# Kernel tuning notes

Hardware: AMD Instinct MI355X
Metric: run time of the kernel (lower is better)

## Reference

```python
import jax, jax.numpy as jnp
import numpy as np

N, M, D = 8192, 8192, 64

def setup_inputs() -> dict:
    key = jax.random.key(0)
    kx, ky = jax.random.split(key)
    x = jax.random.normal(kx, (N, D), dtype=jnp.float32)
    y = jax.random.normal(ky, (M, D), dtype=jnp.float32)
    sigma = jnp.array(1.0, dtype=jnp.float32)
    return {"x": x, "y": y, "sigma": sigma}

def reference(x, y, sigma):
    # Flatten trailing dims (no-op here since inputs are already 2-D).
    x2 = x.reshape(x.shape[0], -1)
    y2 = y.reshape(y.shape[0], -1)
    # Pairwise squared distances via the GEMM trick:
    # |x_i - y_j|^2 = |x_i|^2 + |y_j|^2 - 2 x_i . y_j
    xn = jnp.sum(x2 * x2, axis=1)            # [N]
    yn = jnp.sum(y2 * y2, axis=1)            # [M]
    cross = x2 @ y2.T                         # [N, M]
    sqd = xn[:, None] + yn[None, :] - 2.0 * cross
    sqd = jnp.maximum(sqd, 0.0)               # clamp tiny negatives from fp error
    return jnp.exp(-0.5 * sqd / (sigma * sigma))  # [N, M]
```

## Files before the change

### kernel.cpp

```cpp
#include <hip/hip_runtime.h>
#include <hip/hip_bf16.h>

#define N 8192
#define M 8192
#define D 64

typedef __bf16 bf16x8 __attribute__((ext_vector_type(8)));
typedef float f32x4 __attribute__((ext_vector_type(4)));

__global__ __launch_bounds__(256) void prep_kernel(
    const float* __restrict__ x, const float* __restrict__ y,
    __bf16* __restrict__ xh, __bf16* __restrict__ xl, float* __restrict__ xn,
    __bf16* __restrict__ yh, __bf16* __restrict__ yl, float* __restrict__ yn)
{
    int row  = blockIdx.x * 4 + (threadIdx.x >> 6);
    int lane = threadIdx.x & 63;

    const float* src;
    __bf16 *h, *l;
    float* nrm;
    int r;
    if (row < N) { src = x; h = xh; l = xl; nrm = xn; r = row; }
    else         { src = y; h = yh; l = yl; nrm = yn; r = row - N; }

    float v = src[(size_t)r * D + lane];
    __bf16 hi = (__bf16)v;
    float  lof = v - (float)hi;
    __bf16 lo = (__bf16)lof;

    h[(size_t)r * D + lane] = hi;
    l[(size_t)r * D + lane] = lo;

    float s = v * v;
    #pragma unroll
    for (int off = 32; off; off >>= 1) s += __shfl_down(s, off, 64);
    if (lane == 0) nrm[r] = s;
}

__global__ __launch_bounds__(256) void rbf_kernel(
    const __bf16* __restrict__ xh, const __bf16* __restrict__ xl,
    const float* __restrict__ xn,
    const __bf16* __restrict__ yh, const __bf16* __restrict__ yl,
    const float* __restrict__ yn,
    const float* __restrict__ sig, float* __restrict__ out)
{
    int tid  = threadIdx.x;
    int wave = tid >> 6;
    int lane = tid & 63;
    int quad = lane >> 4;
    int l16  = lane & 15;

    int i_base = blockIdx.y * 128 + (wave >> 1) * 64;
    int j_base = blockIdx.x * 128 + (wave & 1) * 64;

    float s = sig[0];
    float scale = -0.5f / (s * s);

    bf16x8 Bh[4][2], Bl[4][2];
    float ynr[4];
    #pragma unroll
    for (int t = 0; t < 4; ++t) {
        int col = j_base + 4 * l16 + t;
        ynr[t] = yn[col];
        #pragma unroll
        for (int k = 0; k < 2; ++k) {
            int off = col * D + k * 32 + quad * 8;
            Bh[t][k] = *reinterpret_cast<const bf16x8*>(yh + off);
            Bl[t][k] = *reinterpret_cast<const bf16x8*>(yl + off);
        }
    }

    #pragma unroll
    for (int ti = 0; ti < 4; ++ti) {
        int arow = i_base + ti * 16 + l16;
        bf16x8 Ah[2], Al[2];
        #pragma unroll
        for (int k = 0; k < 2; ++k) {
            int off = arow * D + k * 32 + quad * 8;
            Ah[k] = *reinterpret_cast<const bf16x8*>(xh + off);
            Al[k] = *reinterpret_cast<const bf16x8*>(xl + off);
        }

        float xnr[4];
        #pragma unroll
        for (int r = 0; r < 4; ++r)
            xnr[r] = xn[i_base + ti * 16 + quad * 4 + r];

        f32x4 acc[4];
        #pragma unroll
        for (int t = 0; t < 4; ++t) acc[t] = (f32x4){0.f, 0.f, 0.f, 0.f};

        #pragma unroll
        for (int t = 0; t < 4; ++t) {
            #pragma unroll
            for (int k = 0; k < 2; ++k) {
                acc[t] = __builtin_amdgcn_mfma_f32_16x16x32_bf16(Ah[k], Bh[t][k], acc[t], 0, 0, 0);
                acc[t] = __builtin_amdgcn_mfma_f32_16x16x32_bf16(Ah[k], Bl[t][k], acc[t], 0, 0, 0);
                acc[t] = __builtin_amdgcn_mfma_f32_16x16x32_bf16(Al[k], Bh[t][k], acc[t], 0, 0, 0);
            }
        }

        #pragma unroll
        for (int r = 0; r < 4; ++r) {
            int row = i_base + ti * 16 + quad * 4 + r;
            f32x4 v;
            #pragma unroll
            for (int t = 0; t < 4; ++t) {
                float sqd = xnr[r] + ynr[t] - 2.0f * acc[t][r];
                sqd = fmaxf(sqd, 0.0f);
                v[t] = __expf(scale * sqd);
            }
            *reinterpret_cast<f32x4*>(out + (size_t)row * M + j_base + 4 * l16) = v;
        }
    }
}

extern "C" void kernel_launch(void* const* d_in, const int* in_sizes, int n_in,
                              void* d_out, int out_size, void* d_ws, size_t ws_size,
                              hipStream_t stream) {
    const float* x   = (const float*)d_in[0];
    const float* y   = (const float*)d_in[1];
    const float* sig = (const float*)d_in[2];
    float* out = (float*)d_out;

    char* ws = (char*)d_ws;
    __bf16* xh = (__bf16*)(ws);
    __bf16* xl = (__bf16*)(ws + (1u << 20));
    __bf16* yh = (__bf16*)(ws + (2u << 20));
    __bf16* yl = (__bf16*)(ws + (3u << 20));
    float*  xn = (float*) (ws + (4u << 20));
    float*  yn = (float*) (ws + (4u << 20) + (1u << 15));

    prep_kernel<<<(N + M) / 4, 256, 0, stream>>>(x, y, xh, xl, xn, yh, yl, yn);

    dim3 grid(M / 128, N / 128);
    rbf_kernel<<<grid, 256, 0, stream>>>(xh, xl, xn, yh, yl, yn, sig, out);
}
```

Baseline: 291.2 us.

## Pre-swizzle bf16 operands into MFMA fragment order and use nontemporal output stores

```diff
diff --git a/kernel.cpp b/kernel.cpp
--- a/kernel.cpp
+++ b/kernel.cpp
@@ -10,37 +10,56 @@
 
 __global__ __launch_bounds__(256) void prep_kernel(
     const float* __restrict__ x, const float* __restrict__ y,
-    __bf16* __restrict__ xh, __bf16* __restrict__ xl, float* __restrict__ xn,
-    __bf16* __restrict__ yh, __bf16* __restrict__ yl, float* __restrict__ yn)
+    __bf16* __restrict__ xsh, __bf16* __restrict__ xsl, float* __restrict__ xn,
+    __bf16* __restrict__ ysh, __bf16* __restrict__ ysl, float* __restrict__ yn)
 {
-    int row  = blockIdx.x * 4 + (threadIdx.x >> 6);
-    int lane = threadIdx.x & 63;
+    int t   = threadIdx.x;
+    int row = blockIdx.x * 32 + (t >> 3);
+    int c   = t & 7;
 
     const float* src;
-    __bf16 *h, *l;
+    __bf16 *ph, *pl;
     float* nrm;
     int r;
-    if (row < N) { src = x; h = xh; l = xl; nrm = xn; r = row; }
-    else         { src = y; h = yh; l = yl; nrm = yn; r = row - N; }
+    bool isx = row < N;
+    if (isx) { src = x; ph = xsh; pl = xsl; nrm = xn; r = row; }
+    else     { src = y; ph = ysh; pl = ysl; nrm = yn; r = row - N; }
 
-    float v = src[(size_t)r * D + lane];
-    __bf16 hi = (__bf16)v;
-    float  lof = v - (float)hi;
-    __bf16 lo = (__bf16)lof;
+    const float* p = src + (size_t)r * D + c * 8;
+    f32x4 a = *reinterpret_cast<const f32x4*>(p);
+    f32x4 b = *reinterpret_cast<const f32x4*>(p + 4);
+    float v[8] = {a[0], a[1], a[2], a[3], b[0], b[1], b[2], b[3]};
 
-    h[(size_t)r * D + lane] = hi;
-    l[(size_t)r * D + lane] = lo;
+    bf16x8 hv, lv;
+    float s = 0.0f;
+    #pragma unroll
+    for (int i = 0; i < 8; ++i) {
+        float vi = v[i];
+        __bf16 hi = (__bf16)vi;
+        float lof = vi - (float)hi;
+        hv[i] = hi;
+        lv[i] = (__bf16)lof;
+        s += vi * vi;
+    }
+    s += __shfl_down(s, 4);
+    s += __shfl_down(s, 2);
+    s += __shfl_down(s, 1);
 
-    float s = v * v;
-    #pragma unroll
-    for (int off = 32; off; off >>= 1) s += __shfl_down(s, off, 64);
-    if (lane == 0) nrm[r] = s;
+    int g = r >> 6, m = r & 63;
+    int slot;
+    if (isx) slot = ((m >> 4) * 2 + (c >> 2)) * 64 + (c & 3) * 16 + (m & 15);
+    else     slot = ((m & 3)  * 2 + (c >> 2)) * 64 + (c & 3) * 16 + (m >> 2);
+    size_t idx = (size_t)g * 4096 + (size_t)slot * 8;
+
+    *reinterpret_cast<bf16x8*>(ph + idx) = hv;
+    *reinterpret_cast<bf16x8*>(pl + idx) = lv;
+    if (c == 0) nrm[r] = s;
 }
 
 __global__ __launch_bounds__(256) void rbf_kernel(
-    const __bf16* __restrict__ xh, const __bf16* __restrict__ xl,
+    const __bf16* __restrict__ xsh, const __bf16* __restrict__ xsl,
     const float* __restrict__ xn,
-    const __bf16* __restrict__ yh, const __bf16* __restrict__ yl,
+    const __bf16* __restrict__ ysh, const __bf16* __restrict__ ysl,
     const float* __restrict__ yn,
     const float* __restrict__ sig, float* __restrict__ out)
 {
@@ -56,49 +75,43 @@
     float s = sig[0];
     float scale = -0.5f / (s * s);
 
+    const __bf16* pbh = ysh + (size_t)(j_base >> 6) * 4096 + lane * 8;
+    const __bf16* pbl = ysl + (size_t)(j_base >> 6) * 4096 + lane * 8;
     bf16x8 Bh[4][2], Bl[4][2];
-    float ynr[4];
     #pragma unroll
-    for (int t = 0; t < 4; ++t) {
-        int col = j_base + 4 * l16 + t;
-        ynr[t] = yn[col];
+    for (int t = 0; t < 4; ++t)
         #pragma unroll
         for (int k = 0; k < 2; ++k) {
-            int off = col * D + k * 32 + quad * 8;
-            Bh[t][k] = *reinterpret_cast<const bf16x8*>(yh + off);
-            Bl[t][k] = *reinterpret_cast<const bf16x8*>(yl + off);
+            Bh[t][k] = *reinterpret_cast<const bf16x8*>(pbh + (t * 2 + k) * 512);
+            Bl[t][k] = *reinterpret_cast<const bf16x8*>(pbl + (t * 2 + k) * 512);
         }
-    }
+    f32x4 ynv = *reinterpret_cast<const f32x4*>(yn + j_base + 4 * l16);
+
+    const __bf16* pah = xsh + (size_t)(i_base >> 6) * 4096 + lane * 8;
+    const __bf16* pal = xsl + (size_t)(i_base >> 6) * 4096 + lane * 8;
 
     #pragma unroll
     for (int ti = 0; ti < 4; ++ti) {
-        int arow = i_base + ti * 16 + l16;
         bf16x8 Ah[2], Al[2];
         #pragma unroll
         for (int k = 0; k < 2; ++k) {
-            int off = arow * D + k * 32 + quad * 8;
-            Ah[k] = *reinterpret_cast<const bf16x8*>(xh + off);
-            Al[k] = *reinterpret_cast<const bf16x8*>(xl + off);
+            Ah[k] = *reinterpret_cast<const bf16x8*>(pah + (ti * 2 + k) * 512);
+            Al[k] = *reinterpret_cast<const bf16x8*>(pal + (ti * 2 + k) * 512);
         }
-
-        float xnr[4];
-        #pragma unroll
-        for (int r = 0; r < 4; ++r)
-            xnr[r] = xn[i_base + ti * 16 + quad * 4 + r];
+        f32x4 xnv = *reinterpret_cast<const f32x4*>(xn + i_base + ti * 16 + quad * 4);
 
         f32x4 acc[4];
         #pragma unroll
         for (int t = 0; t < 4; ++t) acc[t] = (f32x4){0.f, 0.f, 0.f, 0.f};
 
         #pragma unroll
-        for (int t = 0; t < 4; ++t) {
+        for (int k = 0; k < 2; ++k)
             #pragma unroll
-            for (int k = 0; k < 2; ++k) {
+            for (int t = 0; t < 4; ++t) {
                 acc[t] = __builtin_amdgcn_mfma_f32_16x16x32_bf16(Ah[k], Bh[t][k], acc[t], 0, 0, 0);
                 acc[t] = __builtin_amdgcn_mfma_f32_16x16x32_bf16(Ah[k], Bl[t][k], acc[t], 0, 0, 0);
                 acc[t] = __builtin_amdgcn_mfma_f32_16x16x32_bf16(Al[k], Bh[t][k], acc[t], 0, 0, 0);
             }
-        }
 
         #pragma unroll
         for (int r = 0; r < 4; ++r) {
@@ -106,11 +119,12 @@
             f32x4 v;
             #pragma unroll
             for (int t = 0; t < 4; ++t) {
-                float sqd = xnr[r] + ynr[t] - 2.0f * acc[t][r];
+                float sqd = xnv[r] + ynv[t] - 2.0f * acc[t][r];
                 sqd = fmaxf(sqd, 0.0f);
                 v[t] = __expf(scale * sqd);
             }
-            *reinterpret_cast<f32x4*>(out + (size_t)row * M + j_base + 4 * l16) = v;
+            __builtin_nontemporal_store(
+                v, reinterpret_cast<f32x4*>(out + (size_t)row * M + j_base + 4 * l16));
         }
     }
 }
@@ -124,15 +138,15 @@
     float* out = (float*)d_out;
 
     char* ws = (char*)d_ws;
-    __bf16* xh = (__bf16*)(ws);
-    __bf16* xl = (__bf16*)(ws + (1u << 20));
-    __bf16* yh = (__bf16*)(ws + (2u << 20));
-    __bf16* yl = (__bf16*)(ws + (3u << 20));
-    float*  xn = (float*) (ws + (4u << 20));
-    float*  yn = (float*) (ws + (4u << 20) + (1u << 15));
+    __bf16* xsh = (__bf16*)(ws);
+    __bf16* xsl = (__bf16*)(ws + (1u << 20));
+    __bf16* ysh = (__bf16*)(ws + (2u << 20));
+    __bf16* ysl = (__bf16*)(ws + (3u << 20));
+    float*  xn  = (float*) (ws + (4u << 20));
+    float*  yn  = (float*) (ws + (4u << 20) + (1u << 15));
 
-    prep_kernel<<<(N + M) / 4, 256, 0, stream>>>(x, y, xh, xl, xn, yh, yl, yn);
+    prep_kernel<<<(N + M) / 32, 256, 0, stream>>>(x, y, xsh, xsl, xn, ysh, ysl, yn);
 
     dim3 grid(M / 128, N / 128);
-    rbf_kernel<<<grid, 256, 0, stream>>>(xh, xl, xn, yh, yl, yn, sig, out);
+    rbf_kernel<<<grid, 256, 0, stream>>>(xsh, xsl, xn, ysh, ysl, yn, sig, out);
 }
```

Result: faster. 270.6 us (-7.1%).
